# Performance work log

Hardware: AMD Instinct MI355X
Metric: run time of the kernel (lower is better)

The kernel has to match this reference:

```python
import jax, jax.numpy as jnp
import numpy as np

DIM = 768
HEADS = 12
HEAD_DIM = DIM // HEADS
EPS = 1e-5


def _layernorm(x, w, b):
    # normalize over last axis (head_dim), affine params shape [head_dim]
    mu = jnp.mean(x, axis=-1, keepdims=True)
    var = jnp.mean(jnp.square(x - mu), axis=-1, keepdims=True)
    return (x - mu) * jax.lax.rsqrt(var + EPS) * w + b


def setup_inputs() -> dict:
    key = jax.random.key(0)
    ks = jax.random.split(key, 8)
    B, N, C = 8, 1024, DIM
    s = 1.0 / np.sqrt(C)
    return {
        "x": jax.random.normal(ks[0], (B, N, C), jnp.float32),
        "qkv_w": jax.random.normal(ks[1], (3 * C, C), jnp.float32) * s,
        "qkv_b": jnp.zeros((3 * C,), jnp.float32),
        "qn_w": jnp.ones((HEAD_DIM,), jnp.float32),
        "qn_b": jnp.zeros((HEAD_DIM,), jnp.float32),
        "kn_w": jnp.ones((HEAD_DIM,), jnp.float32),
        "kn_b": jnp.zeros((HEAD_DIM,), jnp.float32),
        "proj_w": jax.random.normal(ks[2], (C, C), jnp.float32) * s,
        "proj_b": jnp.zeros((C,), jnp.float32),
    }


def reference(x, qkv_w, qkv_b, qn_w, qn_b, kn_w, kn_b, proj_w, proj_b):
    B, N, C = x.shape
    H, D = HEADS, HEAD_DIM
    scale = D ** -0.5
    # qkv projection: [B,N,3C] -> [3,B,H,N,D]
    qkv = (x @ qkv_w.T + qkv_b).reshape(B, N, 3, H, D).transpose(2, 0, 3, 1, 4)
    q, k, v = qkv[0], qkv[1], qkv[2]
    q = _layernorm(q, qn_w, qn_b)
    k = _layernorm(k, kn_w, kn_b)
    # attention scores [B,H,N,N]
    attn = jnp.einsum("bhqd,bhkd->bhqk", q, k) * scale
    attn = jax.nn.softmax(attn, axis=-1)
    out = jnp.einsum("bhqk,bhkd->bhqd", attn, v)  # [B,H,N,D]
    out = out.transpose(0, 2, 1, 3).reshape(B, N, C)
    return out @ proj_w.T + proj_b
```

## Files before the change

### kernel.cpp

```cpp
#include <hip/hip_runtime.h>

#define DIM 768
#define HEADS 12
#define HDIM 64
#define B_ 8
#define N_ 1024
#define EPS 1e-5f
#define QPRE 0.18033688f

typedef __bf16 bf16x8 __attribute__((ext_vector_type(8)));
typedef float  f32x4  __attribute__((ext_vector_type(4)));

using u16 = unsigned short;
using u32 = unsigned int;

static __device__ __forceinline__ u16 f2b_rne(float f){
    u32 u = __float_as_uint(f);
    u += 0x7fffu + ((u >> 16) & 1u);
    return (u16)(u >> 16);
}

static __device__ __forceinline__ u32 cvt_pk_bf16(float lo, float hi){
    u32 r;
    asm("v_cvt_pk_bf16_f32 %0, %1, %2" : "=v"(r) : "v"(lo), "v"(hi));
    return r;
}

static __device__ __forceinline__ void gl_lds16(const void* g, void* l){
    __builtin_amdgcn_global_load_lds(
        (const __attribute__((address_space(1))) unsigned int*)g,
        (__attribute__((address_space(3))) unsigned int*)l, 16, 0, 0);
}

__global__ __launch_bounds__(256) void cast_bf16_kernel(
    const float* __restrict__ in, u16* __restrict__ out, int n8)
{
    int i = blockIdx.x * 256 + threadIdx.x;
    if (i >= n8) return;
    const float4* p = (const float4*)in;
    float4 a = p[2*i], b = p[2*i+1];
    uint4 r;
    r.x = (u32)f2b_rne(a.x) | ((u32)f2b_rne(a.y) << 16);
    r.y = (u32)f2b_rne(a.z) | ((u32)f2b_rne(a.w) << 16);
    r.z = (u32)f2b_rne(b.x) | ((u32)f2b_rne(b.y) << 16);
    r.w = (u32)f2b_rne(b.z) | ((u32)f2b_rne(b.w) << 16);
    ((uint4*)out)[i] = r;
}

__global__ __launch_bounds__(256) void qkv_gemm_ln(
    const u16* __restrict__ xb, const u16* __restrict__ wb,
    const float* __restrict__ bias,
    const float* __restrict__ qn_w, const float* __restrict__ qn_b,
    const float* __restrict__ kn_w, const float* __restrict__ kn_b,
    u16* __restrict__ Q, u16* __restrict__ K, u16* __restrict__ VT)
{
    __shared__ __align__(16) unsigned char Asl[2][128*128];
    __shared__ __align__(16) unsigned char Bsl[2][128*128];
    const int t = threadIdx.x;
    const int lane = t & 63, wid = t >> 6;
    const int wr = wid >> 1, wc = wid & 1;
    const int l15 = lane & 15, l4 = lane >> 4;
    const int lr  = lane >> 3;
    const int lcs = ((lane & 7) ^ lr & 7) * 16;
    const int rsw = (l15 & 7) << 4;

    const int b0 = blockIdx.x;
    const int lg = (b0 & 7) * 144 + (b0 >> 3);
    const int col0 = (lg % 18) * 128, row0 = (lg / 18) * 128;

    f32x4 acc[4][4];
    #pragma unroll
    for (int m = 0; m < 4; ++m)
        #pragma unroll
        for (int n = 0; n < 4; ++n) acc[m][n] = f32x4{0.f,0.f,0.f,0.f};

    const unsigned char* aSrc = (const unsigned char*)xb + (size_t)(row0 + lr)*1536 + lcs;
    const unsigned char* bSrc = (const unsigned char*)wb + (size_t)(col0 + lr)*1536 + lcs;

    auto stage = [&](int buf, int k0s){
        #pragma unroll
        for (int c = 0; c < 4; ++c) {
            int rg = wid*32 + c*8;
            gl_lds16(aSrc + (size_t)rg*1536 + k0s*2, Asl[buf] + rg*128);
            gl_lds16(bSrc + (size_t)rg*1536 + k0s*2, Bsl[buf] + rg*128);
        }
    };

    stage(0, 0);

    for (int step = 0; step < 12; ++step) {
        const int cur = step & 1;
        if (step < 11) {
            stage(cur ^ 1, (step + 1) * 64);
            asm volatile("s_waitcnt vmcnt(8)" ::: "memory");
        } else {
            asm volatile("s_waitcnt vmcnt(0)" ::: "memory");
        }
        __builtin_amdgcn_s_barrier();

        #pragma unroll
        for (int s = 0; s < 2; ++s) {
            bf16x8 af[4], bfr[4];
            #pragma unroll
            for (int m = 0; m < 4; ++m)
                af[m] = *(const bf16x8*)(Asl[cur] + (wr*64 + m*16 + l15)*128 + ((l4*16 + s*64) ^ rsw));
            #pragma unroll
            for (int n = 0; n < 4; ++n)
                bfr[n] = *(const bf16x8*)(Bsl[cur] + (wc*64 + n*16 + l15)*128 + ((l4*16 + s*64) ^ rsw));
            #pragma unroll
            for (int m = 0; m < 4; ++m)
                #pragma unroll
                for (int n = 0; n < 4; ++n)
                    acc[m][n] = __builtin_amdgcn_mfma_f32_16x16x32_bf16(af[m], bfr[n], acc[m][n], 0, 0, 0);
        }
        __builtin_amdgcn_s_barrier();
    }

    const int cg0 = col0 + wc*64;
    const int which = cg0 / DIM;
    const int h = (cg0 % DIM) / HDIM;

    float bias_v[4];
    #pragma unroll
    for (int n = 0; n < 4; ++n) bias_v[n] = bias[cg0 + n*16 + l15];
    #pragma unroll
    for (int m = 0; m < 4; ++m)
        #pragma unroll
        for (int n = 0; n < 4; ++n)
            #pragma unroll
            for (int r = 0; r < 4; ++r) acc[m][n][r] += bias_v[n];

    unsigned char* Tw = &Asl[0][0] + wid * 8192;

    if (which < 2) {
        const float* lwp = (which == 0) ? qn_w : kn_w;
        const float* lbp = (which == 0) ? qn_b : kn_b;
        const float qsc = (which == 0) ? QPRE : 1.0f;
        float lw_v[4], lb_v[4];
        #pragma unroll
        for (int n = 0; n < 4; ++n) { lw_v[n] = lwp[n*16 + l15] * qsc; lb_v[n] = lbp[n*16 + l15] * qsc; }

        #pragma unroll
        for (int m = 0; m < 4; ++m)
            #pragma unroll
            for (int r = 0; r < 4; ++r) {
                float s = 0.f, s2 = 0.f;
                #pragma unroll
                for (int n = 0; n < 4; ++n) { float v = acc[m][n][r]; s += v; s2 += v*v; }
                #pragma unroll
                for (int off = 1; off < 16; off <<= 1) {
                    s  += __shfl_xor(s,  off, 64);
                    s2 += __shfl_xor(s2, off, 64);
                }
                float mu  = s * (1.f/64.f);
                float var = s2 * (1.f/64.f) - mu*mu;
                float rs  = rsqrtf(var + EPS);
                #pragma unroll
                for (int n = 0; n < 4; ++n)
                    acc[m][n][r] = (acc[m][n][r] - mu) * rs * lw_v[n] + lb_v[n];
            }

        #pragma unroll
        for (int m = 0; m < 4; ++m)
            #pragma unroll
            for (int n = 0; n < 4; ++n)
                #pragma unroll
                for (int r = 0; r < 4; ++r)
                    *(u16*)(Tw + (m*16 + l4*4 + r)*128 + (n*16 + l15)*2) = f2b_rne(acc[m][n][r]);

        u16* dst = (which == 0) ? Q : K;
        const int tok0 = row0 + wr*64;
        const int b = tok0 >> 10, n0 = tok0 & 1023;
        const size_t bh = (size_t)(b * HEADS + h);
        #pragma unroll
        for (int i = 0; i < 8; ++i) {
            int row = i*8 + (lane >> 3);
            int d0  = (lane & 7) * 8;
            uint4 val = *(const uint4*)(Tw + row*128 + d0*2);
            *(uint4*)(dst + (bh * N_ + n0 + row) * HDIM + d0) = val;
        }
    } else {
        #pragma unroll
        for (int n = 0; n < 4; ++n)
            #pragma unroll
            for (int m = 0; m < 4; ++m)
                #pragma unroll
                for (int r = 0; r < 4; ++r)
                    *(u16*)(Tw + (n*16 + l15)*128 + (m*16 + l4*4 + r)*2) = f2b_rne(acc[m][n][r]);

        const int tok0 = row0 + wr*64;
        const int b = tok0 >> 10, n0v = tok0 & 1023;
        const size_t bh = (size_t)(b * HEADS + h);
        #pragma unroll
        for (int i = 0; i < 8; ++i) {
            int d  = i*8 + (lane >> 3);
            int tk = (lane & 7) * 8;
            uint4 val = *(const uint4*)(Tw + d*128 + tk*2);
            *(uint4*)(VT + (bh * HDIM + d) * N_ + n0v + tk) = val;
        }
    }
}

__global__ __launch_bounds__(256) void attn_mfma(
    const u16* __restrict__ Q, const u16* __restrict__ K,
    const u16* __restrict__ VT, u16* __restrict__ A)
{
    __shared__ __align__(16) unsigned char Ks[2][64*128];
    __shared__ __align__(16) unsigned char Vs[2][64*128];
    __shared__ __align__(16) unsigned char Ps[4*2176];
    const int t = threadIdx.x, lane = t & 63, w = t >> 6;
    const int l15 = lane & 15, l4 = lane >> 4;
    const int lr  = lane >> 3;
    const int lcs = ((lane & 7) ^ lr & 7) * 16;
    const int rsw = (l15 & 7) << 4;
    const int psw = (l15 & 7) << 4;

    const int b0 = blockIdx.x;
    const int lg = (b0 & 7) * 192 + (b0 >> 3);
    const int qt = lg & 15, bh = lg >> 4;
    const size_t base = (size_t)bh * (N_ * HDIM);

    bf16x8 qa[2];
    {
        const unsigned char* qb = (const unsigned char*)(Q + base + (size_t)(qt*64 + w*16 + l15) * HDIM);
        qa[0] = *(const bf16x8*)(qb + l4*16);
        qa[1] = *(const bf16x8*)(qb + l4*16 + 64);
    }

    float l_run = 0.f;
    f32x4 o[4];
    #pragma unroll
    for (int m = 0; m < 4; ++m) o[m] = f32x4{0.f,0.f,0.f,0.f};

    unsigned char* Pw = Ps + w*2176;

    const unsigned char* kSrc = (const unsigned char*)K  + base*2 + (size_t)(w*16 + lr)*128  + lcs;
    const unsigned char* vSrc = (const unsigned char*)VT + base*2 + (size_t)(w*16 + lr)*2048 + lcs;
    unsigned char* kDst0 = Ks[0] + w*16*128;
    unsigned char* vDst0 = Vs[0] + w*16*128;

    auto stage = [&](int buf, int kt2){
        #pragma unroll
        for (int c = 0; c < 2; ++c) {
            gl_lds16(kSrc + (size_t)kt2*8192 + c*1024,  kDst0 + buf*8192 + c*1024);
            gl_lds16(vSrc + kt2*128 + c*16384,          vDst0 + buf*8192 + c*1024);
        }
    };

    stage(0, 0);

    for (int kt = 0; kt < 16; ++kt) {
        const int cur = kt & 1;
        if (kt < 15) {
            stage(cur ^ 1, kt + 1);
            asm volatile("s_waitcnt vmcnt(4)" ::: "memory");
        } else {
            asm volatile("s_waitcnt vmcnt(0)" ::: "memory");
        }
        __builtin_amdgcn_s_barrier();

        f32x4 sv[4];
        #pragma unroll
        for (int n = 0; n < 4; ++n) {
            sv[n] = f32x4{0.f,0.f,0.f,0.f};
            #pragma unroll
            for (int s = 0; s < 2; ++s) {
                bf16x8 kb = *(const bf16x8*)(Ks[cur] + (n*16 + l15)*128 + ((l4*16 + s*64) ^ rsw));
                sv[n] = __builtin_amdgcn_mfma_f32_16x16x32_bf16(kb, qa[s], sv[n], 0, 0, 0);
            }
        }

        #pragma unroll
        for (int n = 0; n < 4; ++n) {
            float p0 = exp2f(sv[n][0]), p1 = exp2f(sv[n][1]);
            float p2 = exp2f(sv[n][2]), p3 = exp2f(sv[n][3]);
            l_run += (p0 + p1) + (p2 + p3);
            uint2 pw;
            pw.x = cvt_pk_bf16(p0, p1);
            pw.y = cvt_pk_bf16(p2, p3);
            *(uint2*)(Pw + l15*128 + ((n*32 + l4*8) ^ psw)) = pw;
        }

        #pragma unroll
        for (int s = 0; s < 2; ++s) {
            bf16x8 pb = *(const bf16x8*)(Pw + l15*128 + ((s*64 + l4*16) ^ psw));
            #pragma unroll
            for (int m = 0; m < 4; ++m) {
                bf16x8 vb = *(const bf16x8*)(Vs[cur] + (m*16 + l15)*128 + ((l4*16 + s*64) ^ rsw));
                o[m] = __builtin_amdgcn_mfma_f32_16x16x32_bf16(vb, pb, o[m], 0, 0, 0);
            }
        }

        __builtin_amdgcn_s_barrier();
    }

    l_run += __shfl_xor(l_run, 16, 64);
    l_run += __shfl_xor(l_run, 32, 64);
    const float inv = 1.f / l_run;

    const int b = bh / HEADS, h = bh % HEADS;
    #pragma unroll
    for (int m = 0; m < 4; ++m)
        #pragma unroll
        for (int r = 0; r < 4; ++r)
            *(u16*)(Pw + l15*132 + (m*16 + l4*4 + r)*2) = f2b_rne(o[m][r] * inv);
    #pragma unroll
    for (int i = 0; i < 2; ++i) {
        int row = i*8 + (lane >> 3);
        int d0  = (lane & 7) * 8;
        uint4 val = *(const uint4*)(Pw + row*132 + d0*2);
        int tok = qt*64 + w*16 + row;
        *(uint4*)(A + (((size_t)b * N_ + tok) * HEADS + h) * HDIM + d0) = val;
    }
}

__global__ __launch_bounds__(256) void proj_gemm(
    const u16* __restrict__ Ab, const u16* __restrict__ wb,
    const float* __restrict__ bias, float* __restrict__ out)
{
    __shared__ __align__(16) unsigned char Asl[2][128*128];
    __shared__ __align__(16) unsigned char Bsl[2][128*128];
    const int t = threadIdx.x;
    const int lane = t & 63, wid = t >> 6;
    const int wr = wid >> 1, wc = wid & 1;
    const int l15 = lane & 15, l4 = lane >> 4;
    const int lr  = lane >> 3;
    const int lcs = ((lane & 7) ^ lr & 7) * 16;
    const int rsw = (l15 & 7) << 4;

    const int b0 = blockIdx.x;
    const int lg = (b0 & 7) * 48 + (b0 >> 3);
    const int col0 = (lg % 6) * 128, row0 = (lg / 6) * 128;

    f32x4 acc[4][4];
    #pragma unroll
    for (int m = 0; m < 4; ++m)
        #pragma unroll
        for (int n = 0; n < 4; ++n) acc[m][n] = f32x4{0.f,0.f,0.f,0.f};

    const unsigned char* aSrc = (const unsigned char*)Ab + (size_t)(row0 + lr)*1536 + lcs;
    const unsigned char* bSrc = (const unsigned char*)wb + (size_t)(col0 + lr)*1536 + lcs;

    auto stage = [&](int buf, int k0s){
        #pragma unroll
        for (int c = 0; c < 4; ++c) {
            int rg = wid*32 + c*8;
            gl_lds16(aSrc + (size_t)rg*1536 + k0s*2, Asl[buf] + rg*128);
            gl_lds16(bSrc + (size_t)rg*1536 + k0s*2, Bsl[buf] + rg*128);
        }
    };

    stage(0, 0);

    for (int step = 0; step < 12; ++step) {
        const int cur = step & 1;
        if (step < 11) {
            stage(cur ^ 1, (step + 1) * 64);
            asm volatile("s_waitcnt vmcnt(8)" ::: "memory");
        } else {
            asm volatile("s_waitcnt vmcnt(0)" ::: "memory");
        }
        __builtin_amdgcn_s_barrier();

        #pragma unroll
        for (int s = 0; s < 2; ++s) {
            bf16x8 af[4], bfr[4];
            #pragma unroll
            for (int m = 0; m < 4; ++m)
                af[m] = *(const bf16x8*)(Asl[cur] + (wr*64 + m*16 + l15)*128 + ((l4*16 + s*64) ^ rsw));
            #pragma unroll
            for (int n = 0; n < 4; ++n)
                bfr[n] = *(const bf16x8*)(Bsl[cur] + (wc*64 + n*16 + l15)*128 + ((l4*16 + s*64) ^ rsw));
            #pragma unroll
            for (int m = 0; m < 4; ++m)
                #pragma unroll
                for (int n = 0; n < 4; ++n)
                    acc[m][n] = __builtin_amdgcn_mfma_f32_16x16x32_bf16(af[m], bfr[n], acc[m][n], 0, 0, 0);
        }
        __builtin_amdgcn_s_barrier();
    }

    float bias_v[4];
    #pragma unroll
    for (int n = 0; n < 4; ++n) bias_v[n] = bias[col0 + wc*64 + n*16 + l15];
    #pragma unroll
    for (int m = 0; m < 4; ++m)
        #pragma unroll
        for (int r = 0; r < 4; ++r) {
            int rg = row0 + wr*64 + m*16 + l4*4 + r;
            #pragma unroll
            for (int n = 0; n < 4; ++n)
                out[(size_t)rg * DIM + col0 + wc*64 + n*16 + l15] = acc[m][n][r] + bias_v[n];
        }
}

extern "C" void kernel_launch(void* const* d_in, const int* in_sizes, int n_in,
                              void* d_out, int out_size, void* d_ws, size_t ws_size,
                              hipStream_t stream)
{
    const float* x      = (const float*)d_in[0];
    const float* qkv_w  = (const float*)d_in[1];
    const float* qkv_b  = (const float*)d_in[2];
    const float* qn_w   = (const float*)d_in[3];
    const float* qn_b   = (const float*)d_in[4];
    const float* kn_w   = (const float*)d_in[5];
    const float* kn_b   = (const float*)d_in[6];
    const float* proj_w = (const float*)d_in[7];
    const float* proj_b = (const float*)d_in[8];
    float* out = (float*)d_out;

    const size_t XE  = (size_t)B_ * N_ * DIM;
    const size_t QWE = (size_t)3 * DIM * DIM;
    const size_t PWE = (size_t)DIM * DIM;

    u16* xb  = (u16*)d_ws;
    u16* qwb = xb  + XE;
    u16* pwb = qwb + QWE;
    u16* Qb  = pwb + PWE;
    u16* Kb  = Qb  + XE;
    u16* VTb = Kb  + XE;
    u16* Ab  = VTb + XE;

    cast_bf16_kernel<<<(int)((XE/8  + 255)/256), 256, 0, stream>>>(x,      xb,  (int)(XE/8));
    cast_bf16_kernel<<<(int)((QWE/8 + 255)/256), 256, 0, stream>>>(qkv_w,  qwb, (int)(QWE/8));
    cast_bf16_kernel<<<(int)((PWE/8 + 255)/256), 256, 0, stream>>>(proj_w, pwb, (int)(PWE/8));

    qkv_gemm_ln<<<dim3(1152), 256, 0, stream>>>(xb, qwb, qkv_b, qn_w, qn_b,
                                                kn_w, kn_b, Qb, Kb, VTb);
    attn_mfma<<<dim3(1536), 256, 0, stream>>>(Qb, Kb, VTb, Ab);
    proj_gemm<<<dim3(384), 256, 0, stream>>>(Ab, pwb, proj_b, out);
}
```

Measured before the change: 143.3 us.

## Load K/V MFMA fragments directly from global memory, dropping LDS staging

Removes the double-buffered LDS staging of K and V tiles, together with its async global-to-LDS copies, waitcnt and block barriers. Each wave now loads its own K and V^T MFMA operand fragments straight from global memory into registers every iteration. This cuts LDS traffic and synchronisation. In exchange, the four waves each fetch the same K/V data redundantly (relying on L1/L2), there is no prefetch overlap, and register pressure rises.

```diff
diff --git a/kernel.cpp b/kernel.cpp
--- a/kernel.cpp
+++ b/kernel.cpp
@@ -205,14 +205,9 @@
     const u16* __restrict__ Q, const u16* __restrict__ K,
     const u16* __restrict__ VT, u16* __restrict__ A)
 {
-    __shared__ __align__(16) unsigned char Ks[2][64*128];
-    __shared__ __align__(16) unsigned char Vs[2][64*128];
     __shared__ __align__(16) unsigned char Ps[4*2176];
     const int t = threadIdx.x, lane = t & 63, w = t >> 6;
     const int l15 = lane & 15, l4 = lane >> 4;
-    const int lr  = lane >> 3;
-    const int lcs = ((lane & 7) ^ lr & 7) * 16;
-    const int rsw = (l15 & 7) << 4;
     const int psw = (l15 & 7) << 4;
 
     const int b0 = blockIdx.x;
@@ -234,41 +229,32 @@
 
     unsigned char* Pw = Ps + w*2176;
 
-    const unsigned char* kSrc = (const unsigned char*)K  + base*2 + (size_t)(w*16 + lr)*128  + lcs;
-    const unsigned char* vSrc = (const unsigned char*)VT + base*2 + (size_t)(w*16 + lr)*2048 + lcs;
-    unsigned char* kDst0 = Ks[0] + w*16*128;
-    unsigned char* vDst0 = Vs[0] + w*16*128;
-
-    auto stage = [&](int buf, int kt2){
-        #pragma unroll
-        for (int c = 0; c < 2; ++c) {
-            gl_lds16(kSrc + (size_t)kt2*8192 + c*1024,  kDst0 + buf*8192 + c*1024);
-            gl_lds16(vSrc + kt2*128 + c*16384,          vDst0 + buf*8192 + c*1024);
-        }
-    };
-
-    stage(0, 0);
+    const unsigned char* kFrag = (const unsigned char*)K  + base*2 + (size_t)l15*128  + l4*16;
+    const unsigned char* vFrag = (const unsigned char*)VT + base*2 + (size_t)l15*2048 + l4*16;
 
     for (int kt = 0; kt < 16; ++kt) {
-        const int cur = kt & 1;
-        if (kt < 15) {
-            stage(cur ^ 1, kt + 1);
-            asm volatile("s_waitcnt vmcnt(4)" ::: "memory");
-        } else {
-            asm volatile("s_waitcnt vmcnt(0)" ::: "memory");
-        }
-        __builtin_amdgcn_s_barrier();
+        bf16x8 kb[4][2];
+        #pragma unroll
+        for (int n = 0; n < 4; ++n)
+            #pragma unroll
+            for (int s = 0; s < 2; ++s)
+                kb[n][s] = *(const bf16x8*)(kFrag + (size_t)(kt*64 + n*16)*128 + s*64);
 
         f32x4 sv[4];
         #pragma unroll
         for (int n = 0; n < 4; ++n) {
             sv[n] = f32x4{0.f,0.f,0.f,0.f};
             #pragma unroll
-            for (int s = 0; s < 2; ++s) {
-                bf16x8 kb = *(const bf16x8*)(Ks[cur] + (n*16 + l15)*128 + ((l4*16 + s*64) ^ rsw));
-                sv[n] = __builtin_amdgcn_mfma_f32_16x16x32_bf16(kb, qa[s], sv[n], 0, 0, 0);
-            }
-        }
+            for (int s = 0; s < 2; ++s)
+                sv[n] = __builtin_amdgcn_mfma_f32_16x16x32_bf16(kb[n][s], qa[s], sv[n], 0, 0, 0);
+        }
+
+        bf16x8 vb[4][2];
+        #pragma unroll
+        for (int m = 0; m < 4; ++m)
+            #pragma unroll
+            for (int s = 0; s < 2; ++s)
+                vb[m][s] = *(const bf16x8*)(vFrag + (size_t)(m*16)*2048 + kt*128 + s*64);
 
         #pragma unroll
         for (int n = 0; n < 4; ++n) {
@@ -285,13 +271,9 @@
         for (int s = 0; s < 2; ++s) {
             bf16x8 pb = *(const bf16x8*)(Pw + l15*128 + ((s*64 + l4*16) ^ psw));
             #pragma unroll
-            for (int m = 0; m < 4; ++m) {
-                bf16x8 vb = *(const bf16x8*)(Vs[cur] + (m*16 + l15)*128 + ((l4*16 + s*64) ^ rsw));
-                o[m] = __builtin_amdgcn_mfma_f32_16x16x32_bf16(vb, pb, o[m], 0, 0, 0);
-            }
-        }
-
-        __builtin_amdgcn_s_barrier();
+            for (int m = 0; m < 4; ++m)
+                o[m] = __builtin_amdgcn_mfma_f32_16x16x32_bf16(vb[m][s], pb, o[m], 0, 0, 0);
+        }
     }
 
     l_run += __shfl_xor(l_run, 16, 64);
```

New measurement: 259.4 us. +81.0%, slower.
